# Kernel tuning notes

Hardware: AMD Instinct MI355X
Metric: run time of the kernel (lower is better)

Reference implementation:

```python
import math
import numpy as np
import jax, jax.numpy as jnp

L_MAX = 3
N_NODES = 16384
C_IN = 128
C_OUT = 128
IRREPS_DIM = (L_MAX + 1) ** 2  # 16 (dims 1+3+5+7, offset of l is l*l)


def _su2_cg(j1, j2, j3):
    """Complex-basis SU(2) Clebsch-Gordan <j1 m1 j2 m2 | j3 m3> (Racah formula)."""
    f = math.factorial
    C = np.zeros((2 * j1 + 1, 2 * j2 + 1, 2 * j3 + 1))
    for m1 in range(-j1, j1 + 1):
        for m2 in range(-j2, j2 + 1):
            m3 = m1 + m2
            if abs(m3) > j3:
                continue
            pref = math.sqrt((2 * j3 + 1) * f(j3 + j1 - j2) * f(j3 - j1 + j2) * f(j1 + j2 - j3) / f(j1 + j2 + j3 + 1))
            pref *= math.sqrt(f(j3 + m3) * f(j3 - m3) * f(j1 - m1) * f(j1 + m1) * f(j2 - m2) * f(j2 + m2))
            s = 0.0
            for k in range(0, j1 + j2 + 1):
                d = [k, j1 + j2 - j3 - k, j1 - m1 - k, j2 + m2 - k, j3 - j2 + m1 + k, j3 - j1 - m2 + k]
                if any(x < 0 for x in d):
                    continue
                s += (-1.0) ** k / (f(d[0]) * f(d[1]) * f(d[2]) * f(d[3]) * f(d[4]) * f(d[5]))
            C[m1 + j1, m2 + j2, m3 + j3] = pref * s
    return C


def _q(l):
    """Real->complex spherical-harmonic change of basis (e3nn convention, incl. (-i)^l)."""
    q = np.zeros((2 * l + 1, 2 * l + 1), dtype=complex)
    r2 = 1.0 / math.sqrt(2.0)
    for m in range(-l, 0):
        q[l + m, l + abs(m)] = r2
        q[l + m, l - abs(m)] = -1j * r2
    q[l, l] = 1.0
    for m in range(1, l + 1):
        q[l + m, l + abs(m)] = (-1) ** m * r2
        q[l + m, l - abs(m)] = 1j * (-1) ** m * r2
    return (-1j) ** l * q


def _real_cg(l1, l2, l3):
    """Real-basis Clebsch-Gordan tensor, shape (2l1+1, 2l2+1, 2l3+1). Real-valued."""
    C = _su2_cg(l1, l2, l3).astype(complex)
    W = np.einsum('ai,bj,ck,abc->ijk', _q(l1), _q(l2), _q(l3), C)
    return np.real(W).astype(np.float32)


# All triangle-allowed coupling paths (l1, l2, l_out); 34 paths for L_MAX=3.
PATHS = [(l1, l2, lo)
         for lo in range(L_MAX + 1)
         for l1 in range(L_MAX + 1)
         for l2 in range(L_MAX + 1)
         if abs(l1 - l2) <= lo <= l1 + l2]
NUM_PATHS = len(PATHS)
_counts = {}
for (_l1, _l2, _lo) in PATHS:
    _counts[_lo] = _counts.get(_lo, 0) + 1
# path_norm: divide each path by sqrt(#paths feeding its output irrep)
PATH_SCALE = [1.0 / math.sqrt(_counts[lo]) for (_, _, lo) in PATHS]
CG = {(l1, l2, lo): _real_cg(l1, l2, lo) for (l1, l2, lo) in PATHS}


def setup_inputs() -> dict:
    key = jax.random.key(0)
    k1, k2, k3 = jax.random.split(key, 3)
    input1 = jax.random.normal(k1, (N_NODES, IRREPS_DIM, C_IN), dtype=jnp.float32)
    input2 = jax.random.normal(k2, (N_NODES, IRREPS_DIM), dtype=jnp.float32)
    # uv-mode weight: (num_paths, channels_in, channels_out); fan-in init std=1/sqrt(C_IN)
    weight = jax.random.normal(k3, (NUM_PATHS, C_IN, C_OUT), dtype=jnp.float32) * (C_IN ** -0.5)
    return {"input1": input1, "input2": input2, "weight": weight}


def _forward(x1, x2, w):
    N = x1.shape[0]
    out = jnp.zeros((N, IRREPS_DIM, w.shape[-1]), dtype=x1.dtype)
    for p, (l1, l2, lo) in enumerate(PATHS):
        Cp = jnp.asarray(CG[(l1, l2, lo)], dtype=x1.dtype)      # (2l1+1, 2l2+1, 2lo+1)
        a = x1[:, l1 * l1:(l1 + 1) ** 2, :]                      # (N, 2l1+1, U)
        b = x2[:, l2 * l2:(l2 + 1) ** 2]                         # (N, 2l2+1)
        t = jnp.einsum('nau,nb,abc->ncu', a, b, Cp)              # (N, 2lo+1, U)
        o = jnp.einsum('ncu,uv->ncv', t, w[p]) * PATH_SCALE[p]   # (N, 2lo+1, V)
        out = out.at[:, lo * lo:(lo + 1) ** 2, :].add(o)
    return out


def reference(input1, input2, weight):
    return _forward(input1, input2, weight)
```

## Files before the change

### kernel.cpp

```cpp
#include <hip/hip_runtime.h>
#include <cstddef>

namespace so3 {

constexpr int IRR  = 16;
constexpr int CIN  = 128;
constexpr int COUT = 128;
constexpr int NP   = 34;
constexpr int NNODES = 16384;
constexpr int MT   = 16;

constexpr int H_L1[NP] = {0,1,2,3, 0,1,1,1,2,2,2,3,3, 0,1,1,1,2,2,2,2,3,3,3, 0,1,1,2,2,2,3,3,3,3};
constexpr int H_L2[NP] = {0,1,2,3, 1,0,1,2,1,2,3,2,3, 2,1,2,3,0,1,2,3,1,2,3, 3,2,3,1,2,3,0,1,2,3};
constexpr int H_LO[NP] = {0,0,0,0, 1,1,1,1,1,1,1,1,1, 2,2,2,2,2,2,2,2,2,2,2, 3,3,3,3,3,3,3,3,3,3};
constexpr int H_START[4] = {0,4,13,24};
constexpr int H_CNT[4]   = {4,9,11,10};

constexpr double cfac(int n){ double r=1.0; for(int i=2;i<=n;++i) r *= (double)i; return r; }
constexpr double csqrt_(double x){
  if(x <= 0.0) return 0.0;
  double r = x < 1.0 ? 1.0 : x;
  for(int i=0;i<60;++i) r = 0.5*(r + x/r);
  return r;
}
constexpr double m1pow(int k){ return (k & 1) ? -1.0 : 1.0; }

struct CD { double re, im; };
constexpr CD cmul(CD a, CD b){ return CD{a.re*b.re - a.im*b.im, a.re*b.im + a.im*b.re}; }

struct CGDense { double v[7][7][7]; };
constexpr CGDense su2_cg(int j1,int j2,int j3){
  CGDense C{};
  for(int m1=-j1;m1<=j1;++m1){
    for(int m2=-j2;m2<=j2;++m2){
      int m3 = m1+m2;
      if(m3 < -j3 || m3 > j3) continue;
      double pref = csqrt_((2*j3+1) * cfac(j3+j1-j2)*cfac(j3-j1+j2)*cfac(j1+j2-j3)/cfac(j1+j2+j3+1));
      pref *= csqrt_(cfac(j3+m3)*cfac(j3-m3)*cfac(j1-m1)*cfac(j1+m1)*cfac(j2-m2)*cfac(j2+m2));
      double s = 0.0;
      for(int k=0;k<=j1+j2;++k){
        int d0=k, d1=j1+j2-j3-k, d2=j1-m1-k, d3=j2+m2-k, d4=j3-j2+m1+k, d5=j3-j1-m2+k;
        if(d0<0||d1<0||d2<0||d3<0||d4<0||d5<0) continue;
        s += m1pow(k)/(cfac(d0)*cfac(d1)*cfac(d2)*cfac(d3)*cfac(d4)*cfac(d5));
      }
      C.v[m1+j1][m2+j2][m3+j3] = pref*s;
    }
  }
  return C;
}

struct QMat { CD v[7][7]; };
constexpr QMat qmat(int l){
  QMat q{};
  const double r2 = 1.0/csqrt_(2.0);
  for(int m=-l;m<0;++m){
    q.v[l+m][l-m] = CD{r2, 0.0};
    q.v[l+m][l+m] = CD{0.0, -r2};
  }
  q.v[l][l] = CD{1.0, 0.0};
  for(int m=1;m<=l;++m){
    double sgn = m1pow(m);
    q.v[l+m][l+m] = CD{sgn*r2, 0.0};
    q.v[l+m][l-m] = CD{0.0, sgn*r2};
  }
  CD ph = CD{1.0, 0.0};
  int lm = l & 3;
  if(lm==1) ph = CD{0.0,-1.0};
  else if(lm==2) ph = CD{-1.0,0.0};
  else if(lm==3) ph = CD{0.0, 1.0};
  for(int i=0;i<2*l+1;++i)
    for(int j=0;j<2*l+1;++j)
      q.v[i][j] = cmul(q.v[i][j], ph);
  return q;
}

struct RealCG { double v[7][7][7]; };
constexpr RealCG real_cg(int l1,int l2,int l3){
  RealCG W{};
  const CGDense C = su2_cg(l1,l2,l3);
  const QMat q1 = qmat(l1), q2 = qmat(l2), q3 = qmat(l3);
  for(int i=0;i<2*l1+1;++i){
    int alist[2] = {i, 2*l1-i};
    int na = (alist[1]==alist[0]) ? 1 : 2;
    for(int j=0;j<2*l2+1;++j){
      int blist[2] = {j, 2*l2-j};
      int nb = (blist[1]==blist[0]) ? 1 : 2;
      for(int k=0;k<2*l3+1;++k){
        int clist[2] = {k, 2*l3-k};
        int nc = (clist[1]==clist[0]) ? 1 : 2;
        double re = 0.0;
        for(int ai=0;ai<na;++ai) for(int bi=0;bi<nb;++bi) for(int ci=0;ci<nc;++ci){
          int a=alist[ai], b=blist[bi], c=clist[ci];
          double cc = C.v[a][b][c];
          if(cc == 0.0) continue;
          CD t = cmul(cmul(q1.v[a][i], q2.v[b][j]), q3.v[c][k]);
          re += t.re * cc;
        }
        W.v[i][j][k] = re;
      }
    }
  }
  return W;
}

#define DECL_CG(n,a,b,c) constexpr RealCG CGP##n = real_cg(a,b,c);
DECL_CG(0,0,0,0)  DECL_CG(1,1,1,0)  DECL_CG(2,2,2,0)  DECL_CG(3,3,3,0)
DECL_CG(4,0,1,1)  DECL_CG(5,1,0,1)  DECL_CG(6,1,1,1)  DECL_CG(7,1,2,1)
DECL_CG(8,2,1,1)  DECL_CG(9,2,2,1)  DECL_CG(10,2,3,1) DECL_CG(11,3,2,1)
DECL_CG(12,3,3,1) DECL_CG(13,0,2,2) DECL_CG(14,1,1,2) DECL_CG(15,1,2,2)
DECL_CG(16,1,3,2) DECL_CG(17,2,0,2) DECL_CG(18,2,1,2) DECL_CG(19,2,2,2)
DECL_CG(20,2,3,2) DECL_CG(21,3,1,2) DECL_CG(22,3,2,2) DECL_CG(23,3,3,2)
DECL_CG(24,0,3,3) DECL_CG(25,1,2,3) DECL_CG(26,1,3,3) DECL_CG(27,2,1,3)
DECL_CG(28,2,2,3) DECL_CG(29,2,3,3) DECL_CG(30,3,0,3) DECL_CG(31,3,1,3)
DECL_CG(32,3,2,3) DECL_CG(33,3,3,3)
#undef DECL_CG

struct CGTable { float v[NP][7][7][7]; };
constexpr CGTable pack_cg(){
  const RealCG arr[NP] = {CGP0,CGP1,CGP2,CGP3,CGP4,CGP5,CGP6,CGP7,CGP8,CGP9,
                          CGP10,CGP11,CGP12,CGP13,CGP14,CGP15,CGP16,CGP17,CGP18,CGP19,
                          CGP20,CGP21,CGP22,CGP23,CGP24,CGP25,CGP26,CGP27,CGP28,CGP29,
                          CGP30,CGP31,CGP32,CGP33};
  CGTable t{};
  for(int p=0;p<NP;++p)
    for(int i=0;i<7;++i) for(int j=0;j<7;++j) for(int k=0;k<7;++k)
      t.v[p][i][j][k] = (float)arr[p].v[i][j][k];
  return t;
}

constexpr float PATH_SC[4] = {
  (float)(1.0/csqrt_((double)H_CNT[0])), (float)(1.0/csqrt_((double)H_CNT[1])),
  (float)(1.0/csqrt_((double)H_CNT[2])), (float)(1.0/csqrt_((double)H_CNT[3]))
};

}

constexpr so3::CGTable CG_HOST = so3::pack_cg();

typedef __attribute__((ext_vector_type(8))) short bhalf8;
typedef __attribute__((ext_vector_type(4))) float floatx4;

__device__ __forceinline__ unsigned f2bf(float f){
  unsigned u = __builtin_bit_cast(unsigned, f);
  return (u + 0x7fffu + ((u>>16)&1u)) >> 16;
}

#define SO3_BAR() do{ __builtin_amdgcn_sched_barrier(0); \
  asm volatile("s_waitcnt lgkmcnt(0)" ::: "memory"); \
  __builtin_amdgcn_s_barrier(); \
  asm volatile("" ::: "memory"); \
  __builtin_amdgcn_sched_barrier(0); }while(0)

template<int P, int C, int A, int B>
__device__ __forceinline__ float cg_dot(const float* __restrict__ x2r)
{
  using namespace so3;
  constexpr int n2 = 2*H_L2[P] + 1;
  if constexpr (B >= n2) { (void)x2r; return 0.f; }
  else {
    constexpr float w = CG_HOST.v[P][A][B][C] * PATH_SC[H_LO[P]];
    float r = cg_dot<P, C, A, B+1>(x2r);
    if constexpr (w != 0.0f) r += w * x2r[B];
    return r;
  }
}

template<int P, int S, int SEND>
__device__ __forceinline__ void stage_a_slots(const int ca,
    float* __restrict__ gout, const float* __restrict__ x2r, const int n)
{
  using namespace so3;
  if constexpr (S < SEND) {
    constexpr int n1 = 2*H_L1[P] + 1;
    constexpr int c = S / n1, a = S % n1;
    if (ca == S) gout[(c*16 + n)*8 + a] = cg_dot<P, c, a, 0>(x2r);
    stage_a_slots<P, S+1, SEND>(ca, gout, x2r, n);
  }
}

template<int P>
__device__ __forceinline__ void stage_a(const int tid, float* __restrict__ gout,
                                        const float* __restrict__ x2s)
{
  using namespace so3;
  constexpr int n1 = 2*H_L1[P] + 1;
  constexpr int NS = (2*H_LO[P] + 1) * n1;
  const int n  = tid & 15;
  const int ca = tid >> 4;
  const float* x2r = x2s + n*17 + H_L2[P]*H_L2[P];
  stage_a_slots<P, 0, (NS < 32 ? NS : 32)>(ca, gout, x2r, n);
  if constexpr (NS > 32)
    stage_a_slots<P, 32, NS>(ca + 32, gout, x2r, n);
}

template<int LO, int PP, int AOFF, int NIRR>
__device__ __forceinline__ void path_iter(const int tid, const long n0,
    const float* __restrict__ x1, unsigned short* __restrict__ Tsh,
    float* __restrict__ gsh, const float* __restrict__ x2s,
    const unsigned short* __restrict__ wT,
    floatx4 (&acc)[NIRR], bhalf8 (&bfrag)[4], float4 (&xf)[7])
{
  using namespace so3;
  constexpr int NR  = 2*LO + 1;
  constexpr int CNT = H_CNT[LO];
  constexpr int TS  = 7*16*128;
  constexpr int GS  = 7*16*8;
  if constexpr (PP > CNT) { return; }
  else {
    const int lane = tid & 63, wv = tid >> 6, lr = lane & 15, lg = lane >> 4;
    const int bn = tid >> 5, u4 = tid & 31;

    if constexpr (PP > 0) {
      constexpr int p = H_START[LO] + PP - 1;
      const unsigned short* wp = wT + p*16384 + (wv*16 + lr)*128 + lg*8;
      #pragma unroll
      for (int ks = 0; ks < 4; ++ks)
        bfrag[ks] = *(const bhalf8*)(wp + ks*32);
    }

    if constexpr (PP < CNT) {
      constexpr int p  = H_START[LO] + PP;
      constexpr int l1 = H_L1[p];
      constexpr bool newg = (PP == 0) || (H_L1[p - 1] != l1);
      if constexpr (newg) {
        constexpr int n1 = 2*l1 + 1;
        const float* xp = x1 + ((size_t)(n0 + bn)*IRR + l1*l1)*CIN + u4*4;
        #pragma unroll
        for (int a = 0; a < n1; ++a)
          xf[a] = *(const float4*)(xp + a*CIN);
      }
    }

    if constexpr (PP + 1 < CNT) {
      stage_a<H_START[LO] + PP + 1>(tid, gsh + ((PP+1)&1)*GS, x2s);
    }

    if constexpr (PP < CNT) {
      constexpr int p  = H_START[LO] + PP;
      constexpr int l1 = H_L1[p]; constexpr int n1 = 2*l1 + 1;
      const float* gin = gsh + (PP&1)*GS;
      char* Tbase = (char*)Tsh + (PP&1)*(TS*2);
      #pragma unroll
      for (int c = 0; c < NR; ++c) {
        const float* g8 = gin + (c*16 + bn)*8;
        float garr[8];
        const float4 ga = *(const float4*)(g8);
        garr[0]=ga.x; garr[1]=ga.y; garr[2]=ga.z; garr[3]=ga.w;
        if constexpr (n1 > 4) {
          const float4 gb = *(const float4*)(g8 + 4);
          garr[4]=gb.x; garr[5]=gb.y; garr[6]=gb.z; garr[7]=gb.w;
        }
        float t0=0.f, t1=0.f, t2=0.f, t3=0.f;
        #pragma unroll
        for (int a = 0; a < n1; ++a) {
          const float4 xa = xf[a];
          t0 += garr[a]*xa.x; t1 += garr[a]*xa.y;
          t2 += garr[a]*xa.z; t3 += garr[a]*xa.w;
        }
        uint2 o;
        o.x = f2bf(t0) | (f2bf(t1) << 16);
        o.y = f2bf(t2) | (f2bf(t3) << 16);
        const unsigned byte = ((unsigned)(((c*16 + bn)*128 + u4*4)*2)) ^ ((unsigned)((bn & 7) << 4));
        *(uint2*)(Tbase + byte) = o;
      }
    }

    if constexpr (PP > 0) {
      const char* Tbase = (const char*)Tsh + ((PP-1)&1)*(TS*2);
      const unsigned xsw = (unsigned)((lr & 7) << 4);
      #pragma unroll
      for (int c = 0; c < NR; ++c) {
        #pragma unroll
        for (int ks = 0; ks < 4; ++ks) {
          const unsigned byte = ((unsigned)((c*16 + lr)*256) + (unsigned)(ks*64 + lg*16)) ^ xsw;
          bhalf8 av = *(const bhalf8*)(Tbase + byte);
          acc[AOFF + c] = __builtin_amdgcn_mfma_f32_16x16x32_bf16(
              av, bfrag[ks], acc[AOFF + c], 0, 0, 0);
        }
      }
    }

    SO3_BAR();
    path_iter<LO, PP+1, AOFF, NIRR>(tid, n0, x1, Tsh, gsh, x2s, wT, acc, bfrag, xf);
  }
}

template<int LOA, int LOB>
__global__ __launch_bounds__(512, 4)
void so3_pair(const float* __restrict__ x1, const float* __restrict__ x2,
              const unsigned short* __restrict__ wT, float* __restrict__ out)
{
  using namespace so3;
  constexpr int NRA = 2*LOA + 1, NRB = 2*LOB + 1, NIRR = NRA + NRB;
  __shared__ __align__(16) char smem[57344 + 7168 + 1152];
  unsigned short* Tsh = (unsigned short*)smem;
  float* gsh = (float*)(smem + 57344);
  float* x2s = (float*)(smem + 57344 + 7168);

  const int tid = threadIdx.x;
  const long n0 = (long)blockIdx.x * MT;

  if (tid < 256) x2s[(tid >> 4)*17 + (tid & 15)] = x2[n0*16 + tid];
  __syncthreads();

  floatx4 acc[NIRR];
  #pragma unroll
  for (int i = 0; i < NIRR; ++i) acc[i] = (floatx4){0.f,0.f,0.f,0.f};
  bhalf8 bfrag[4];
  float4 xf[7];

  stage_a<H_START[LOA]>(tid, gsh, x2s);
  __syncthreads();
  path_iter<LOA, 0, 0, NIRR>(tid, n0, x1, Tsh, gsh, x2s, wT, acc, bfrag, xf);
  __syncthreads();
  stage_a<H_START[LOB]>(tid, gsh, x2s);
  __syncthreads();
  path_iter<LOB, 0, NRA, NIRR>(tid, n0, x1, Tsh, gsh, x2s, wT, acc, bfrag, xf);
  __syncthreads();

  float* epi = (float*)smem;
  const int lane = tid & 63, wv = tid >> 6, lr = lane & 15, lg = lane >> 4;
  const int v = wv*16 + lr;
  #pragma unroll
  for (int ch = 0; ch < 2; ++ch) {
    if (ch) __syncthreads();
    #pragma unroll
    for (int ii = 0; ii < 4; ++ii) {
      #pragma unroll
      for (int r = 0; r < 4; ++r)
        epi[(ii*16 + lg*4 + r)*132 + v] = acc[ch*4 + ii][r];
    }
    __syncthreads();
    #pragma unroll
    for (int j = 0; j < 4; ++j) {
      const int k   = tid + j*512;
      const int row = k >> 5, c4 = k & 31;
      const int n   = row >> 2, ii = row & 3;
      const int idx = ch*4 + ii;
      const int gi  = (idx < NRA) ? (LOA*LOA + idx) : (LOB*LOB + idx - NRA);
      const float4 val = *(const float4*)(epi + (ii*16 + n)*132 + c4*4);
      *(float4*)(out + ((n0 + n)*16 + gi)*128 + c4*4) = val;
    }
  }
}

__global__ void prep_wT(const float* __restrict__ w, unsigned short* __restrict__ wT)
{
  const int idx = blockIdx.x*256 + threadIdx.x;
  if (idx >= 34*128*128) return;
  const int p = idx >> 14, rem = idx & 16383, u = rem >> 7, v = rem & 127;
  wT[(p << 14) + (v << 7) + u] = (unsigned short)f2bf(w[idx]);
}

extern "C" void kernel_launch(void* const* d_in, const int* in_sizes, int n_in,
                              void* d_out, int out_size, void* d_ws, size_t ws_size,
                              hipStream_t stream)
{
  (void)in_sizes; (void)n_in; (void)out_size; (void)ws_size;
  const float* x1 = (const float*)d_in[0];
  const float* x2 = (const float*)d_in[1];
  const float* w  = (const float*)d_in[2];
  float* out = (float*)d_out;

  unsigned short* wT = (unsigned short*)d_ws;
  prep_wT<<<dim3(2176), dim3(256), 0, stream>>>(w, wT);
  so3_pair<0,3><<<dim3(so3::NNODES / so3::MT), dim3(512), 0, stream>>>(x1, x2, wT, out);
  so3_pair<1,2><<<dim3(so3::NNODES / so3::MT), dim3(512), 0, stream>>>(x1, x2, wT, out);
}
```

Baseline: 308.0 us.

## Interleave paths of both output irreps per pipeline step to cut barriers

Instead of running all paths for one output irrep and then the other, each pipeline step now processes one path from each irrep group that share the same l1. This cuts the number of barrier-separated iterations and lets one x1 load feed two paths. Shared memory buffers grow to hold up to 8 rows per stage, and a second weight fragment set is held in registers, which raises register and LDS pressure and may affect occupancy.

After: 347.6 us. +12.9%, slower.

```diff
diff --git a/kernel.cpp b/kernel.cpp
--- a/kernel.cpp
+++ b/kernel.cpp
@@ -133,6 +133,20 @@
   (float)(1.0/csqrt_((double)H_CNT[2])), (float)(1.0/csqrt_((double)H_CNT[3]))
 };
 
+constexpr int NIV_K[2] = {10, 11};
+constexpr int IVA[2][11] = {
+  {0, 1, 26, 2, 28, 29, 3, 31, 32, 33, -1},
+  {4, 5, 6, 7, 8, 9, 10, 20, 11, 12, 23}
+};
+constexpr int IVB[2][11] = {
+  {24, 25, -1, 27, -1, -1, 30, -1, -1, -1, -1},
+  {13, 14, 15, 16, 17, 18, 19, -1, 21, 22, -1}
+};
+constexpr int nr_of(int P){ return P < 0 ? 0 : 2*H_LO[P] + 1; }
+constexpr int aoff_of(int LOA, int P){
+  return P < 0 ? 0 : (H_LO[P] == LOA ? 0 : 2*LOA + 1);
+}
+
 }
 
 constexpr so3::CGTable CG_HOST = so3::pack_cg();
@@ -193,35 +207,87 @@
     stage_a_slots<P, 32, NS>(ca + 32, gout, x2r, n);
 }
 
-template<int LO, int PP, int AOFF, int NIRR>
-__device__ __forceinline__ void path_iter(const int tid, const long n0,
+template<int P, int R0>
+__device__ __forceinline__ void stage_b(const int bn, const int u4,
+    const float* __restrict__ gin, char* __restrict__ Tbase,
+    const float4 (&xf)[7])
+{
+  using namespace so3;
+  constexpr int NR = 2*H_LO[P] + 1;
+  constexpr int n1 = 2*H_L1[P] + 1;
+  #pragma unroll
+  for (int c = 0; c < NR; ++c) {
+    const float* g8 = gin + (c*16 + bn)*8;
+    float garr[8];
+    const float4 ga = *(const float4*)(g8);
+    garr[0]=ga.x; garr[1]=ga.y; garr[2]=ga.z; garr[3]=ga.w;
+    if constexpr (n1 > 4) {
+      const float4 gb = *(const float4*)(g8 + 4);
+      garr[4]=gb.x; garr[5]=gb.y; garr[6]=gb.z; garr[7]=gb.w;
+    }
+    float t0=0.f, t1=0.f, t2=0.f, t3=0.f;
+    #pragma unroll
+    for (int a = 0; a < n1; ++a) {
+      const float4 xa = xf[a];
+      t0 += garr[a]*xa.x; t1 += garr[a]*xa.y;
+      t2 += garr[a]*xa.z; t3 += garr[a]*xa.w;
+    }
+    uint2 o;
+    o.x = f2bf(t0) | (f2bf(t1) << 16);
+    o.y = f2bf(t2) | (f2bf(t3) << 16);
+    const unsigned byte = ((unsigned)((((R0 + c)*16 + bn)*128 + u4*4)*2)) ^ ((unsigned)((bn & 7) << 4));
+    *(uint2*)(Tbase + byte) = o;
+  }
+}
+
+template<int P, int R0, int AOFF>
+__device__ __forceinline__ void mfma_path(const char* __restrict__ Tbase,
+    const bhalf8 (&bf)[4], floatx4 (&acc)[8],
+    const int lr, const int lg, const unsigned xsw)
+{
+  using namespace so3;
+  constexpr int NR = 2*H_LO[P] + 1;
+  #pragma unroll
+  for (int c = 0; c < NR; ++c) {
+    #pragma unroll
+    for (int ks = 0; ks < 4; ++ks) {
+      const unsigned byte = ((unsigned)(((R0 + c)*16 + lr)*256) + (unsigned)(ks*64 + lg*16)) ^ xsw;
+      bhalf8 av = *(const bhalf8*)(Tbase + byte);
+      acc[AOFF + c] = __builtin_amdgcn_mfma_f32_16x16x32_bf16(
+          av, bf[ks], acc[AOFF + c], 0, 0, 0);
+    }
+  }
+}
+
+template<int KID, int LOA, int I>
+__device__ __forceinline__ void q_iter(const int tid, const long n0,
     const float* __restrict__ x1, unsigned short* __restrict__ Tsh,
     float* __restrict__ gsh, const float* __restrict__ x2s,
     const unsigned short* __restrict__ wT,
-    floatx4 (&acc)[NIRR], bhalf8 (&bfrag)[4], float4 (&xf)[7])
-{
-  using namespace so3;
-  constexpr int NR  = 2*LO + 1;
-  constexpr int CNT = H_CNT[LO];
-  constexpr int TS  = 7*16*128;
-  constexpr int GS  = 7*16*8;
-  if constexpr (PP > CNT) { return; }
+    floatx4 (&acc)[8], bhalf8 (&bfA)[4], bhalf8 (&bfB)[4], float4 (&xf)[7])
+{
+  using namespace so3;
+  constexpr int NIV = NIV_K[KID];
+  constexpr int TSB = 8*16*128*2;
+  constexpr int GS  = 8*16*8;
+  if constexpr (I > NIV) { return; }
   else {
     const int lane = tid & 63, wv = tid >> 6, lr = lane & 15, lg = lane >> 4;
     const int bn = tid >> 5, u4 = tid & 31;
-
-    if constexpr (PP > 0) {
-      constexpr int p = H_START[LO] + PP - 1;
-      const unsigned short* wp = wT + p*16384 + (wv*16 + lr)*128 + lg*8;
+    const unsigned xsw = (unsigned)((lr & 7) << 4);
+
+    if constexpr (I > 0) {
+      constexpr int PAp = IVA[KID][I-1];
+      const unsigned short* wp = wT + PAp*16384 + (wv*16 + lr)*128 + lg*8;
       #pragma unroll
       for (int ks = 0; ks < 4; ++ks)
-        bfrag[ks] = *(const bhalf8*)(wp + ks*32);
-    }
-
-    if constexpr (PP < CNT) {
-      constexpr int p  = H_START[LO] + PP;
-      constexpr int l1 = H_L1[p];
-      constexpr bool newg = (PP == 0) || (H_L1[p - 1] != l1);
+        bfA[ks] = *(const bhalf8*)(wp + ks*32);
+    }
+
+    if constexpr (I < NIV) {
+      constexpr int PA = IVA[KID][I];
+      constexpr int l1 = H_L1[PA];
+      constexpr bool newg = (I == 0) || (H_L1[IVA[KID][I-1]] != l1);
       if constexpr (newg) {
         constexpr int n1 = 2*l1 + 1;
         const float* xp = x1 + ((size_t)(n0 + bn)*IRR + l1*l1)*CIN + u4*4;
@@ -231,71 +297,61 @@
       }
     }
 
-    if constexpr (PP + 1 < CNT) {
-      stage_a<H_START[LO] + PP + 1>(tid, gsh + ((PP+1)&1)*GS, x2s);
-    }
-
-    if constexpr (PP < CNT) {
-      constexpr int p  = H_START[LO] + PP;
-      constexpr int l1 = H_L1[p]; constexpr int n1 = 2*l1 + 1;
-      const float* gin = gsh + (PP&1)*GS;
-      char* Tbase = (char*)Tsh + (PP&1)*(TS*2);
-      #pragma unroll
-      for (int c = 0; c < NR; ++c) {
-        const float* g8 = gin + (c*16 + bn)*8;
-        float garr[8];
-        const float4 ga = *(const float4*)(g8);
-        garr[0]=ga.x; garr[1]=ga.y; garr[2]=ga.z; garr[3]=ga.w;
-        if constexpr (n1 > 4) {
-          const float4 gb = *(const float4*)(g8 + 4);
-          garr[4]=gb.x; garr[5]=gb.y; garr[6]=gb.z; garr[7]=gb.w;
-        }
-        float t0=0.f, t1=0.f, t2=0.f, t3=0.f;
+    if constexpr (I + 1 < NIV) {
+      constexpr int PA1 = IVA[KID][I+1];
+      constexpr int PB1 = IVB[KID][I+1];
+      float* gout = gsh + ((I+1)&1)*GS;
+      stage_a<PA1>(tid, gout, x2s);
+      if constexpr (PB1 >= 0)
+        stage_a<PB1>(tid, gout + nr_of(PA1)*16*8, x2s);
+    }
+
+    if constexpr (I > 0) {
+      constexpr int PBp = IVB[KID][I-1];
+      if constexpr (PBp >= 0) {
+        const unsigned short* wp = wT + PBp*16384 + (wv*16 + lr)*128 + lg*8;
         #pragma unroll
-        for (int a = 0; a < n1; ++a) {
-          const float4 xa = xf[a];
-          t0 += garr[a]*xa.x; t1 += garr[a]*xa.y;
-          t2 += garr[a]*xa.z; t3 += garr[a]*xa.w;
-        }
-        uint2 o;
-        o.x = f2bf(t0) | (f2bf(t1) << 16);
-        o.y = f2bf(t2) | (f2bf(t3) << 16);
-        const unsigned byte = ((unsigned)(((c*16 + bn)*128 + u4*4)*2)) ^ ((unsigned)((bn & 7) << 4));
-        *(uint2*)(Tbase + byte) = o;
+        for (int ks = 0; ks < 4; ++ks)
+          bfB[ks] = *(const bhalf8*)(wp + ks*32);
       }
     }
 
-    if constexpr (PP > 0) {
-      const char* Tbase = (const char*)Tsh + ((PP-1)&1)*(TS*2);
-      const unsigned xsw = (unsigned)((lr & 7) << 4);
-      #pragma unroll
-      for (int c = 0; c < NR; ++c) {
-        #pragma unroll
-        for (int ks = 0; ks < 4; ++ks) {
-          const unsigned byte = ((unsigned)((c*16 + lr)*256) + (unsigned)(ks*64 + lg*16)) ^ xsw;
-          bhalf8 av = *(const bhalf8*)(Tbase + byte);
-          acc[AOFF + c] = __builtin_amdgcn_mfma_f32_16x16x32_bf16(
-              av, bfrag[ks], acc[AOFF + c], 0, 0, 0);
-        }
-      }
+    if constexpr (I < NIV) {
+      constexpr int PA = IVA[KID][I];
+      constexpr int PB = IVB[KID][I];
+      const float* gin = gsh + (I&1)*GS;
+      char* Tb = (char*)Tsh + (I&1)*TSB;
+      stage_b<PA, 0>(bn, u4, gin, Tb, xf);
+      if constexpr (PB >= 0)
+        stage_b<PB, nr_of(PA)>(bn, u4, gin + nr_of(PA)*16*8, Tb, xf);
+    }
+
+    if constexpr (I > 0) {
+      constexpr int PAp = IVA[KID][I-1];
+      constexpr int PBp = IVB[KID][I-1];
+      const char* Tb = (const char*)Tsh + ((I-1)&1)*TSB;
+      mfma_path<PAp, 0, aoff_of(LOA, PAp)>(Tb, bfA, acc, lr, lg, xsw);
+      if constexpr (PBp >= 0)
+        mfma_path<PBp, nr_of(PAp), aoff_of(LOA, PBp)>(Tb, bfB, acc, lr, lg, xsw);
     }
 
     SO3_BAR();
-    path_iter<LO, PP+1, AOFF, NIRR>(tid, n0, x1, Tsh, gsh, x2s, wT, acc, bfrag, xf);
-  }
-}
-
-template<int LOA, int LOB>
+    q_iter<KID, LOA, I+1>(tid, n0, x1, Tsh, gsh, x2s, wT, acc, bfA, bfB, xf);
+  }
+}
+
+template<int KID, int LOA, int LOB>
 __global__ __launch_bounds__(512, 4)
 void so3_pair(const float* __restrict__ x1, const float* __restrict__ x2,
               const unsigned short* __restrict__ wT, float* __restrict__ out)
 {
   using namespace so3;
-  constexpr int NRA = 2*LOA + 1, NRB = 2*LOB + 1, NIRR = NRA + NRB;
-  __shared__ __align__(16) char smem[57344 + 7168 + 1152];
+  constexpr int NRA = 2*LOA + 1, NRB = 2*LOB + 1;
+  constexpr int GS = 8*16*8;
+  __shared__ __align__(16) char smem[65536 + 2*GS*4 + 1088];
   unsigned short* Tsh = (unsigned short*)smem;
-  float* gsh = (float*)(smem + 57344);
-  float* x2s = (float*)(smem + 57344 + 7168);
+  float* gsh = (float*)(smem + 65536);
+  float* x2s = (float*)(smem + 65536 + 2*GS*4);
 
   const int tid = threadIdx.x;
   const long n0 = (long)blockIdx.x * MT;
@@ -303,20 +359,22 @@
   if (tid < 256) x2s[(tid >> 4)*17 + (tid & 15)] = x2[n0*16 + tid];
   __syncthreads();
 
-  floatx4 acc[NIRR];
+  floatx4 acc[8];
   #pragma unroll
-  for (int i = 0; i < NIRR; ++i) acc[i] = (floatx4){0.f,0.f,0.f,0.f};
-  bhalf8 bfrag[4];
+  for (int i = 0; i < 8; ++i) acc[i] = (floatx4){0.f,0.f,0.f,0.f};
+  bhalf8 bfA[4], bfB[4];
   float4 xf[7];
 
-  stage_a<H_START[LOA]>(tid, gsh, x2s);
+  {
+    constexpr int PA0 = IVA[KID][0];
+    constexpr int PB0 = IVB[KID][0];
+    stage_a<PA0>(tid, gsh, x2s);
+    if constexpr (PB0 >= 0)
+      stage_a<PB0>(tid, gsh + nr_of(PA0)*16*8, x2s);
+  }
   __syncthreads();
-  path_iter<LOA, 0, 0, NIRR>(tid, n0, x1, Tsh, gsh, x2s, wT, acc, bfrag, xf);
-  __syncthreads();
-  stage_a<H_START[LOB]>(tid, gsh, x2s);
-  __syncthreads();
-  path_iter<LOB, 0, NRA, NIRR>(tid, n0, x1, Tsh, gsh, x2s, wT, acc, bfrag, xf);
-  __syncthreads();
+
+  q_iter<KID, LOA, 0>(tid, n0, x1, Tsh, gsh, x2s, wT, acc, bfA, bfB, xf);
 
   float* epi = (float*)smem;
   const int lane = tid & 63, wv = tid >> 6, lr = lane & 15, lg = lane >> 4;
@@ -364,6 +422,6 @@
 
   unsigned short* wT = (unsigned short*)d_ws;
   prep_wT<<<dim3(2176), dim3(256), 0, stream>>>(w, wT);
-  so3_pair<0,3><<<dim3(so3::NNODES / so3::MT), dim3(512), 0, stream>>>(x1, x2, wT, out);
-  so3_pair<1,2><<<dim3(so3::NNODES / so3::MT), dim3(512), 0, stream>>>(x1, x2, wT, out);
-}
+  so3_pair<0, 0, 3><<<dim3(so3::NNODES / so3::MT), dim3(512), 0, stream>>>(x1, x2, wT, out);
+  so3_pair<1, 1, 2><<<dim3(so3::NNODES / so3::MT), dim3(512), 0, stream>>>(x1, x2, wT, out);
+}
```
